# Performance work log

Measured on AMD Instinct MI355X. Metric: run time of the kernel, lower is better.

## Reference

```python
import jax, jax.numpy as jnp
import numpy as np

B, Lq, Lk, D, H = 8, 1024, 1024, 1024, 16
HD = D // H  # 64


def rotate_half(x):
    x1, x2 = jnp.split(x, 2, axis=-1)
    return jnp.concatenate([-x2, x1], axis=-1)


def setup_inputs() -> dict:
    key = jax.random.key(0)
    ks = jax.random.split(key, 16)
    inv_freq = 1.0 / (10000.0 ** (np.arange(0, HD, 2, dtype=np.float32) / HD))
    pos = np.arange(Lk, dtype=np.float32)
    ang = pos[:, None] * inv_freq[None, :]              # [Lk, HD/2]
    emb = np.concatenate([ang, ang], axis=-1)           # [Lk, HD]
    rope_cos = jnp.broadcast_to(jnp.asarray(np.cos(emb)), (B, Lk, HD))
    rope_sin = jnp.broadcast_to(jnp.asarray(np.sin(emb)), (B, Lk, HD))
    w = lambda k: jax.random.normal(k, (D, D), jnp.float32) * 0.02
    return {
        "query": jax.random.normal(ks[0], (B, Lq, D), jnp.float32),
        "key": jax.random.normal(ks[1], (B, Lk, D), jnp.float32),
        "value": jax.random.normal(ks[2], (B, Lk, D), jnp.float32),
        "Wq": w(ks[3]), "bq": jnp.zeros((D,), jnp.float32),
        "Wk": w(ks[4]), "bk": jnp.zeros((D,), jnp.float32),
        "Wv": w(ks[5]), "bv": jnp.zeros((D,), jnp.float32),
        "Wg": w(ks[6]), "bg": jnp.ones((D,), jnp.float32),
        "Wo": w(ks[7]), "bo": jnp.zeros((D,), jnp.float32),
        "rope_cos": rope_cos,
        "rope_sin": rope_sin,
        "key_padding_mask": jnp.zeros((B, Lk), bool),  # True = padded
    }


def reference(query, key, value, Wq, bq, Wk, bk, Wv, bv, Wg, bg, Wo, bo,
              rope_cos, rope_sin, key_padding_mask):
    b, lq, d = query.shape
    lk = key.shape[1]
    h, hd = H, d // H

    def heads(x, L):  # [B,L,D] -> [B,H,L,hd]
        return x.reshape(b, L, h, hd).transpose(0, 2, 1, 3)

    Q = heads(query @ Wq.T + bq, lq)
    K = heads(key @ Wk.T + bk, lk)
    V = heads(value @ Wv.T + bv, lk)

    def rope(x, cos, sin):
        L = x.shape[2]
        c = cos[:, None, :L, :]
        s = sin[:, None, :L, :]
        return x * c + rotate_half(x) * s

    K = rope(K, rope_cos, rope_sin)
    Q = rope(Q, rope_cos, rope_sin)  # rope_on_q=True, q uses same cos/sin

    scale = 1.0 / np.sqrt(hd)
    scores = jnp.einsum('bhqd,bhkd->bhqk', Q, K) * scale
    valid = ~key_padding_mask                     # [B,Lk], True = attend
    scores = jnp.where(valid[:, None, None, :], scores, jnp.float32(-1e30))
    attn = jax.nn.softmax(scores, axis=-1)
    out = jnp.einsum('bhqk,bhkd->bhqd', attn, V)  # [B,H,Lq,hd]
    out = jnp.nan_to_num(out, nan=0.0)
    out = out.transpose(0, 2, 1, 3).reshape(b, lq, d)
    gate = jax.nn.sigmoid(query @ Wg.T + bg)
    out = (out * gate) @ Wo.T + bo
    return out
```

## Files before the change

### kernel.cpp

```cpp
#include <hip/hip_runtime.h>

using ushort  = unsigned short;
using bf16x8  = __attribute__((ext_vector_type(8))) __bf16;
using bf16x4  = __attribute__((ext_vector_type(4))) __bf16;
using ushort8 = __attribute__((ext_vector_type(8))) unsigned short;
using f32x4   = __attribute__((ext_vector_type(4))) float;
using float4v = __attribute__((ext_vector_type(4))) float;

__device__ __forceinline__ float bf2f(ushort u) {
    union { unsigned int i; float f; } v; v.i = ((unsigned int)u) << 16; return v.f;
}
__device__ __forceinline__ ushort f2bf(float f) {
    union { float f; unsigned int i; } v; v.f = f;
    unsigned int r = v.i + 0x7FFFu + ((v.i >> 16) & 1u);
    return (ushort)(r >> 16);
}
__device__ __forceinline__ bf16x8 ld8(const ushort* p) {
    return __builtin_bit_cast(bf16x8, *(const ushort8*)p);
}
__device__ __forceinline__ void glds16(const void* g, void* l) {
    __builtin_amdgcn_global_load_lds(
        (const __attribute__((address_space(1))) unsigned int*)g,
        (__attribute__((address_space(3))) unsigned int*)l, 16, 0, 0);
}

__global__ void sniff_kernel(const ushort* __restrict__ q, int* __restrict__ flag) {
    const int lane = threadIdx.x;
    float mx = 0.0f;
    for (int i = lane; i < 512; i += 64) {
        float v = bf2f(q[2 * i]);
        mx = fmaxf(mx, fabsf(v));
    }
#pragma unroll
    for (int off = 32; off >= 1; off >>= 1) mx = fmaxf(mx, __shfl_xor(mx, off, 64));
    if (lane == 0) *flag = (mx > 1.0e6f) ? 1 : 0;
}

__device__ __forceinline__ void cvt8(const void* src, ushort* dst, int i, bool f32m) {
    if (f32m) {
        const float4v a = ((const float4v*)src)[2 * i];
        const float4v b = ((const float4v*)src)[2 * i + 1];
        bf16x8 o;
#pragma unroll
        for (int j = 0; j < 4; ++j) { o[j] = (__bf16)a[j]; o[j + 4] = (__bf16)b[j]; }
        ((ushort8*)dst)[i] = __builtin_bit_cast(ushort8, o);
    } else {
        ((ushort8*)dst)[i] = ((const ushort8*)src)[i];
    }
}

__global__ __launch_bounds__(256) void cvt_qkv(
    const void* __restrict__ s0, const void* __restrict__ s1, const void* __restrict__ s2,
    ushort* __restrict__ d0, ushort* __restrict__ d1, ushort* __restrict__ d2,
    const int* __restrict__ flag)
{
    const bool f32m = (*flag != 0);
    const int seg = blockIdx.x >> 11;
    const void* src = seg == 0 ? s0 : (seg == 1 ? s1 : s2);
    ushort*    dst = seg == 0 ? d0 : (seg == 1 ? d1 : d2);
    for (int i = (blockIdx.x & 2047) * 256 + threadIdx.x; i < 1048576; i += 2048 * 256)
        cvt8(src, dst, i, f32m);
}
__global__ __launch_bounds__(256) void cvt_w5(
    const void* __restrict__ s0, const void* __restrict__ s1, const void* __restrict__ s2,
    const void* __restrict__ s3, const void* __restrict__ s4,
    ushort* __restrict__ d0, ushort* __restrict__ d1, ushort* __restrict__ d2,
    ushort* __restrict__ d3, ushort* __restrict__ d4,
    const int* __restrict__ flag)
{
    const bool f32m = (*flag != 0);
    const int seg = blockIdx.x >> 9;
    const void* src = seg == 0 ? s0 : seg == 1 ? s1 : seg == 2 ? s2 : seg == 3 ? s3 : s4;
    ushort*    dst = seg == 0 ? d0 : seg == 1 ? d1 : seg == 2 ? d2 : seg == 3 ? d3 : d4;
    cvt8(src, dst, (blockIdx.x & 511) * 256 + threadIdx.x, f32m);
}

template<int EPI, int ABF16, int WBF16, int OUTF>
__global__ __launch_bounds__(256) void gemm_bt(
    const void* __restrict__ A, const void* __restrict__ W,
    const void* __restrict__ bias,
    const void* __restrict__ rc, const void* __restrict__ rs,
    void* __restrict__ C, const int* __restrict__ flag)
{
    constexpr int Kd = 1024, Nd = 1024;
    const bool f32m = (*flag != 0);
    const bool af32 = f32m && !ABF16;
    const bool wf32 = f32m && !WBF16;

    const int tid  = threadIdx.x;
    const int swz  = (blockIdx.x & 7) * 64 + (blockIdx.x >> 3);
    const int nb   = swz & 7;
    const int mb   = swz >> 3;
    const int wave = tid >> 6;
    const int lane = tid & 63;
    const int quad = lane >> 4;
    const int l16  = lane & 15;
    const int wr   = wave >> 1;
    const int wc   = wave & 1;

    __shared__ __align__(16) ushort As[2][128 * 32];
    __shared__ __align__(16) ushort Bs[2][128 * 32];

    const int arow0 = mb * 128;
    const int brow0 = nb * 128;

    auto ldregs = [&](float4v r[4], const float* src, int row0, int k0) {
#pragma unroll
        for (int j = 0; j < 2; ++j) {
            const int c = j * 256 + tid;
            const float* gp = src + (size_t)(row0 + (c >> 2)) * Kd + k0 + (c & 3) * 8;
            r[2 * j]     = *(const float4v*)gp;
            r[2 * j + 1] = *(const float4v*)(gp + 4);
        }
    };
    auto cvtwr = [&](ushort* lds, const float4v r[4]) {
#pragma unroll
        for (int j = 0; j < 2; ++j) {
            const int c = j * 256 + tid;
            bf16x8 o;
#pragma unroll
            for (int i = 0; i < 4; ++i) {
                o[i]     = (__bf16)r[2 * j][i];
                o[i + 4] = (__bf16)r[2 * j + 1][i];
            }
            *(ushort8*)&lds[c * 8] = __builtin_bit_cast(ushort8, o);
        }
    };
    auto stage16 = [&](ushort* lds, const ushort* src, int row0, int k0) {
#pragma unroll
        for (int j = 0; j < 2; ++j) {
            const int c = j * 256 + tid;
            glds16(src + (size_t)(row0 + (c >> 2)) * Kd + k0 + (c & 3) * 8, &lds[c * 8]);
        }
    };

    {
        float4v t[4];
        if (af32) { ldregs(t, (const float*)A, arow0, 0); cvtwr(As[0], t); }
        else      stage16(As[0], (const ushort*)A, arow0, 0);
        if (wf32) { ldregs(t, (const float*)W, brow0, 0); cvtwr(Bs[0], t); }
        else      stage16(Bs[0], (const ushort*)W, brow0, 0);
    }

    f32x4 acc[4][4] = {};
    int cur = 0;
    for (int kt = 0; kt < 32; ++kt) {
        __syncthreads();
        const bool pf = (kt < 31);
        const int  kn = (kt + 1) * 32;
        float4v ra[4], rb[4];
        if (pf) {
            if (af32) ldregs(ra, (const float*)A, arow0, kn);
            else      stage16(As[cur ^ 1], (const ushort*)A, arow0, kn);
            if (wf32) ldregs(rb, (const float*)W, brow0, kn);
            else      stage16(Bs[cur ^ 1], (const ushort*)W, brow0, kn);
        }
        bf16x8 fa[4], fb[4];
#pragma unroll
        for (int mi = 0; mi < 4; ++mi)
            fa[mi] = ld8(&As[cur][(wr * 64 + mi * 16 + l16) * 32 + quad * 8]);
#pragma unroll
        for (int ni = 0; ni < 4; ++ni)
            fb[ni] = ld8(&Bs[cur][(wc * 64 + ni * 16 + l16) * 32 + quad * 8]);
#pragma unroll
        for (int mi = 0; mi < 4; ++mi)
#pragma unroll
            for (int ni = 0; ni < 4; ++ni)
                acc[mi][ni] = __builtin_amdgcn_mfma_f32_16x16x32_bf16(fa[mi], fb[ni], acc[mi][ni], 0, 0, 0);
        if (pf) {
            if (af32) cvtwr(As[cur ^ 1], ra);
            if (wf32) cvtwr(Bs[cur ^ 1], rb);
        }
        cur ^= 1;
    }

    const bool of32 = OUTF && f32m;
    const int colbase = nb * 128 + wc * 64;
    float bv[4];
#pragma unroll
    for (int ni = 0; ni < 4; ++ni) {
        const int cg = colbase + ni * 16 + l16;
        bv[ni] = f32m ? ((const float*)bias)[cg] : bf2f(((const ushort*)bias)[cg]);
    }
    const int rowb = mb * 128 + wr * 64 + quad * 4;
#pragma unroll
    for (int mi = 0; mi < 4; ++mi) {
#pragma unroll
        for (int r = 0; r < 4; ++r) {
            const int rowg = rowb + mi * 16 + r;
            float v[4];
#pragma unroll
            for (int ni = 0; ni < 4; ++ni) v[ni] = acc[mi][ni][r] + bv[ni];
            if constexpr (EPI == 1 || EPI == 3) {
#pragma unroll
                for (int t = 0; t < 2; ++t) {
                    const size_t ci = (size_t)rowg * 64 + t * 16 + l16;
                    const float c = f32m ? ((const float*)rc)[ci] : bf2f(((const ushort*)rc)[ci]);
                    const float s = f32m ? ((const float*)rs)[ci] : bf2f(((const ushort*)rs)[ci]);
                    const float x1 = v[t], x2 = v[t + 2];
                    v[t]     = x1 * c - x2 * s;
                    v[t + 2] = x2 * c + x1 * s;
                }
                if constexpr (EPI == 3) {
#pragma unroll
                    for (int t = 0; t < 4; ++t) v[t] *= 0.125f;
                }
            } else if constexpr (EPI == 2) {
#pragma unroll
                for (int t = 0; t < 4; ++t) v[t] = 1.0f / (1.0f + __expf(-v[t]));
            }
#pragma unroll
            for (int ni = 0; ni < 4; ++ni) {
                const size_t idx = (size_t)rowg * Nd + colbase + ni * 16 + l16;
                if (of32) ((float*)C)[idx] = v[ni];
                else      ((ushort*)C)[idx] = f2bf(v[ni]);
            }
        }
    }
}

__global__ __launch_bounds__(256) void transpose_vh(
    const ushort* __restrict__ Vp, ushort* __restrict__ Vt)
{
    const int bb = blockIdx.x >> 8;
    const int pr = (blockIdx.x >> 4) & 15;
    const int cr = blockIdx.x & 15;
    __shared__ ushort t[64 * 65];
    const int tid = threadIdx.x;
    {
        const int r = tid >> 3, c8 = (tid & 7) * 8;
#pragma unroll
        for (int hh = 0; hh < 2; ++hh) {
            const int rr = r + hh * 32;
            const ushort8 v = *(const ushort8*)(Vp + ((size_t)(bb * 1024 + pr * 64 + rr)) * 1024 + cr * 64 + c8);
#pragma unroll
            for (int i = 0; i < 8; ++i) t[rr * 65 + c8 + i] = v[i];
        }
    }
    __syncthreads();
    {
        const int c = tid >> 2, p0 = (tid & 3) * 16;
        ushort8 o0, o1;
#pragma unroll
        for (int i = 0; i < 8; ++i) {
            o0[i] = t[(p0 + i) * 65 + c];
            o1[i] = t[(p0 + 8 + i) * 65 + c];
        }
        ushort* dst = Vt + ((size_t)(bb * 1024 + cr * 64 + c)) * 1024 + pr * 64 + p0;
        *(ushort8*)dst       = o0;
        *(ushort8*)(dst + 8) = o1;
    }
}

__global__ __launch_bounds__(512) void attn_kernel(
    const ushort* __restrict__ Qp, const ushort* __restrict__ Kp,
    const ushort* __restrict__ Vt, const ushort* __restrict__ G,
    const unsigned char* __restrict__ mask, ushort* __restrict__ O)
{
    const int swz = (blockIdx.x & 7) * 64 + (blockIdx.x >> 3);
    const int qb = swz & 3;
    const int h  = (swz >> 2) & 15;
    const int b  = swz >> 6;
    const int tid  = threadIdx.x;
    const int wave = tid >> 6;
    const int lane = tid & 63;
    const int quad = lane >> 4;
    const int l16  = lane & 15;
    const size_t Dm = 1024;

    __shared__ __align__(16) ushort Ks[2][64 * 64];
    __shared__ __align__(16) ushort Vs[2][64 * 64];
    __shared__ __align__(16) ushort Ps[8][16 * 72];
    __shared__ __align__(16) unsigned char Ms[1024];

    const int q0 = qb * 256 + wave * 32;
    bf16x8 qa[2][2];
#pragma unroll
    for (int u = 0; u < 2; ++u) {
        const ushort* Qb = Qp + ((size_t)b * 1024 + q0 + u * 16 + l16) * Dm + h * 64 + quad * 8;
        qa[u][0] = ld8(Qb);
        qa[u][1] = ld8(Qb + 32);
    }
    const ushort* Kbase = Kp + ((size_t)b * 1024) * Dm + h * 64;
    const ushort* Vbase = Vt + ((size_t)b * 1024 + h * 64) * 1024;

    auto stageK = [&](ushort* lds, int k0) {
        const int row = tid >> 3;
        const int col8 = (tid & 7) ^ (row & 7);
        glds16(Kbase + (size_t)(k0 + row) * Dm + col8 * 8, &lds[tid * 8]);
    };
    auto stageV = [&](ushort* lds, int k0) {
        const int row = tid >> 3;
        const int col8 = (tid & 7) ^ (row & 7);
        glds16(Vbase + (size_t)row * 1024 + k0 + col8 * 8, &lds[tid * 8]);
    };

    stageK(Ks[0], 0);
    stageV(Vs[0], 0);
    if (tid < 256)
        ((unsigned int*)Ms)[tid] = ((const unsigned int*)(mask + (size_t)b * 1024))[tid];
    __syncthreads();
    bool anym;
    {
        const unsigned long long* M8 = (const unsigned long long*)Ms;
        anym = __any((M8[lane] | M8[lane + 64]) != 0ULL);
    }

    float m_r[2] = { -3.0e38f, -3.0e38f };
    float l_r[2] = { 0.0f, 0.0f };
    f32x4 o[2][4] = {};

    int cur = 0;
    for (int kt = 0; kt < 16; ++kt) {
        __syncthreads();
        if (kt < 15) {
            stageK(Ks[cur ^ 1], (kt + 1) * 64);
            stageV(Vs[cur ^ 1], (kt + 1) * 64);
        }
        const int k0 = kt * 64;
        bf16x8 kf0[4], kf1[4];
#pragma unroll
        for (int ct = 0; ct < 4; ++ct) {
            const int row = ct * 16 + l16;
            kf0[ct] = ld8(&Ks[cur][row * 64 + ((quad)     ^ (row & 7)) * 8]);
            kf1[ct] = ld8(&Ks[cur][row * 64 + ((4 + quad) ^ (row & 7)) * 8]);
        }
        f32x4 s[2][4] = {};
        __builtin_amdgcn_s_setprio(1);
#pragma unroll
        for (int u = 0; u < 2; ++u)
#pragma unroll
            for (int ct = 0; ct < 4; ++ct) {
                s[u][ct] = __builtin_amdgcn_mfma_f32_16x16x32_bf16(kf0[ct], qa[u][0], s[u][ct], 0, 0, 0);
                s[u][ct] = __builtin_amdgcn_mfma_f32_16x16x32_bf16(kf1[ct], qa[u][1], s[u][ct], 0, 0, 0);
            }
        __builtin_amdgcn_s_setprio(0);
        bf16x8 vf[4][2];
#pragma unroll
        for (int t = 0; t < 4; ++t) {
            const int row = t * 16 + l16;
#pragma unroll
            for (int kk = 0; kk < 2; ++kk)
                vf[t][kk] = ld8(&Vs[cur][row * 64 + (((kk * 4 + quad) ^ (row & 7))) * 8]);
        }
#pragma unroll
        for (int u = 0; u < 2; ++u) {
            float sv[4][4];
#pragma unroll
            for (int ct = 0; ct < 4; ++ct)
#pragma unroll
                for (int r = 0; r < 4; ++r) sv[ct][r] = s[u][ct][r];
            if (anym) {
#pragma unroll
                for (int ct = 0; ct < 4; ++ct) {
                    const unsigned int mb4 = *(const unsigned int*)&Ms[k0 + ct * 16 + quad * 4];
#pragma unroll
                    for (int r = 0; r < 4; ++r)
                        if ((mb4 >> (8 * r)) & 0xffu) sv[ct][r] = -1e30f;
                }
            }
            float mxv = sv[0][0];
#pragma unroll
            for (int ct = 0; ct < 4; ++ct)
#pragma unroll
                for (int r = 0; r < 4; ++r) mxv = fmaxf(mxv, sv[ct][r]);
            mxv = fmaxf(mxv, __shfl_xor(mxv, 16, 64));
            mxv = fmaxf(mxv, __shfl_xor(mxv, 32, 64));
            if (__any(mxv > m_r[u] + 8.0f)) {
                const float mnew  = fmaxf(m_r[u], mxv);
                const float alpha = __expf(m_r[u] - mnew);
                l_r[u] *= alpha;
                m_r[u]  = mnew;
#pragma unroll
                for (int r = 0; r < 4; ++r) {
                    const float ar = __shfl(alpha, quad * 4 + r, 64);
#pragma unroll
                    for (int t = 0; t < 4; ++t) o[u][t][r] *= ar;
                }
            }
            float ls = 0.0f;
            bf16x4 w[4];
#pragma unroll
            for (int ct = 0; ct < 4; ++ct)
#pragma unroll
                for (int r = 0; r < 4; ++r) {
                    const float pv = __expf(sv[ct][r] - m_r[u]);
                    ls += pv;
                    w[ct][r] = (__bf16)pv;
                }
            l_r[u] += ls;
#pragma unroll
            for (int ct = 0; ct < 4; ++ct)
                *(bf16x4*)&Ps[wave][l16 * 72 + ct * 16 + quad * 4] = w[ct];
            asm volatile("s_waitcnt lgkmcnt(0)" ::: "memory");
            __builtin_amdgcn_sched_barrier(0);
            const bf16x8 pa0 = ld8(&Ps[wave][l16 * 72 + quad * 8]);
            const bf16x8 pa1 = ld8(&Ps[wave][l16 * 72 + 32 + quad * 8]);
            __builtin_amdgcn_s_setprio(1);
#pragma unroll
            for (int t = 0; t < 4; ++t) {
                o[u][t] = __builtin_amdgcn_mfma_f32_16x16x32_bf16(pa0, vf[t][0], o[u][t], 0, 0, 0);
                o[u][t] = __builtin_amdgcn_mfma_f32_16x16x32_bf16(pa1, vf[t][1], o[u][t], 0, 0, 0);
            }
            __builtin_amdgcn_s_setprio(0);
        }
        cur ^= 1;
    }
#pragma unroll
    for (int u = 0; u < 2; ++u) {
        float lt = l_r[u];
        lt += __shfl_xor(lt, 16, 64);
        lt += __shfl_xor(lt, 32, 64);
        const int rowg0 = b * 1024 + q0 + u * 16 + quad * 4;
#pragma unroll
        for (int r = 0; r < 4; ++r) {
            const float inv = 1.0f / __shfl(lt, quad * 4 + r, 64);
#pragma unroll
            for (int t = 0; t < 4; ++t) {
                const size_t idx = (size_t)(rowg0 + r) * Dm + h * 64 + t * 16 + l16;
                O[idx] = f2bf(o[u][t][r] * inv * bf2f(G[idx]));
            }
        }
    }
}

extern "C" void kernel_launch(void* const* d_in, const int* in_sizes, int n_in,
                              void* d_out, int out_size, void* d_ws, size_t ws_size,
                              hipStream_t stream)
{
    const void* query = d_in[0];
    const void* key   = d_in[1];
    const void* value = d_in[2];
    const void* Wq    = d_in[3];
    const void* bq    = d_in[4];
    const void* Wk    = d_in[5];
    const void* bk    = d_in[6];
    const void* Wv    = d_in[7];
    const void* bv    = d_in[8];
    const void* Wg    = d_in[9];
    const void* bg    = d_in[10];
    const void* Wo    = d_in[11];
    const void* bo    = d_in[12];
    const void* rc    = d_in[13];
    const void* rs    = d_in[14];
    const unsigned char* mask = (const unsigned char*)d_in[15];

    char* ws = (char*)d_ws;
    const size_t MB = (size_t)1 << 20;
    const size_t MB16 = 16 * MB;
    const bool big = ws_size >= 139 * MB;

    ushort* Qp = (ushort*)(ws);
    ushort* Kp = (ushort*)(ws + 1 * MB16);
    ushort* Vp = (ushort*)(ws + 2 * MB16);
    ushort* Gt = (ushort*)(ws + 3 * MB16);
    ushort* Vt = (ushort*)(ws + 4 * MB16);
    ushort* Ag = (ushort*)(ws + 2 * MB16);
    int*  flag = (int*)(ws + (big ? 138 * MB : 5 * MB16));

    const dim3 gb(512), gt(256);
    hipLaunchKernelGGL(sniff_kernel, dim3(1), dim3(64), 0, stream, (const ushort*)query, flag);

    if (big) {
        ushort* qbf = (ushort*)(ws + 80 * MB);
        ushort* kbf = (ushort*)(ws + 96 * MB);
        ushort* vbf = (ushort*)(ws + 112 * MB);
        ushort* wb[5];
        for (int i = 0; i < 5; ++i) wb[i] = (ushort*)(ws + 128 * MB + (size_t)i * 2 * MB);

        hipLaunchKernelGGL(cvt_qkv, dim3(3 * 2048), dim3(256), 0, stream,
                           query, key, value, qbf, kbf, vbf, flag);
        hipLaunchKernelGGL(cvt_w5, dim3(5 * 512), dim3(256), 0, stream,
                           Wq, Wk, Wv, Wg, Wo, wb[0], wb[1], wb[2], wb[3], wb[4], flag);

        hipLaunchKernelGGL((gemm_bt<3,1,1,0>), gb, gt, 0, stream, qbf, wb[0], bq, rc, rs, Qp, flag);
        hipLaunchKernelGGL((gemm_bt<1,1,1,0>), gb, gt, 0, stream, kbf, wb[1], bk, rc, rs, Kp, flag);
        hipLaunchKernelGGL((gemm_bt<0,1,1,0>), gb, gt, 0, stream, vbf, wb[2], bv, rc, rs, Vp, flag);
        hipLaunchKernelGGL((gemm_bt<2,1,1,0>), gb, gt, 0, stream, qbf, wb[3], bg, rc, rs, Gt, flag);

        hipLaunchKernelGGL(transpose_vh, dim3(2048), dim3(256), 0, stream, Vp, Vt);
        hipLaunchKernelGGL(attn_kernel,  dim3(512), dim3(512), 0, stream, Qp, Kp, Vt, Gt, mask, Ag);

        hipLaunchKernelGGL((gemm_bt<0,1,1,1>), gb, gt, 0, stream, Ag, wb[4], bo, rc, rs, d_out, flag);
    } else {
        hipLaunchKernelGGL((gemm_bt<3,0,0,0>), gb, gt, 0, stream, query, Wq, bq, rc, rs, Qp, flag);
        hipLaunchKernelGGL((gemm_bt<1,0,0,0>), gb, gt, 0, stream, key,   Wk, bk, rc, rs, Kp, flag);
        hipLaunchKernelGGL((gemm_bt<0,0,0,0>), gb, gt, 0, stream, value, Wv, bv, rc, rs, Vp, flag);
        hipLaunchKernelGGL((gemm_bt<2,0,0,0>), gb, gt, 0, stream, query, Wg, bg, rc, rs, Gt, flag);

        hipLaunchKernelGGL(transpose_vh, dim3(2048), dim3(256), 0, stream, Vp, Vt);
        hipLaunchKernelGGL(attn_kernel,  dim3(512), dim3(512), 0, stream, Qp, Kp, Vt, Gt, mask, Ag);

        hipLaunchKernelGGL((gemm_bt<0,1,0,1>), gb, gt, 0, stream, Ag, Wo, bo, rc, rs, d_out, flag);
    }
}
```

Before: 411.4 us.

## Fuse Q/K/V/gate projections into one GEMM launch and batch PV MFMAs

Replaces four separate projection GEMM launches with a single 2048-block kernel over a contiguous concatenated weight buffer, picking input, bias, epilogue and output per column segment. This fills the machine with one larger grid and removes launch gaps and tail effects between GEMMs. Separately, the attention kernel now writes P for both 16-row sub-tiles to a doubled LDS buffer and issues one wait and one batch of PV MFMAs, cutting waitcnt stalls. The attention change costs extra LDS and register pressure, and the fused GEMM adds runtime segment branches in its epilogue.

```diff
diff --git a/kernel.cpp b/kernel.cpp
--- a/kernel.cpp
+++ b/kernel.cpp
@@ -214,6 +214,119 @@
                 const size_t idx = (size_t)rowg * Nd + colbase + ni * 16 + l16;
                 if (of32) ((float*)C)[idx] = v[ni];
                 else      ((ushort*)C)[idx] = f2bf(v[ni]);
+            }
+        }
+    }
+}
+
+__global__ __launch_bounds__(256) void gemm_qkvg(
+    const ushort* __restrict__ qbf, const ushort* __restrict__ kbf,
+    const ushort* __restrict__ vbf, const ushort* __restrict__ Wcat,
+    const void* __restrict__ bq, const void* __restrict__ bk,
+    const void* __restrict__ bv_, const void* __restrict__ bg,
+    const void* __restrict__ rc, const void* __restrict__ rs,
+    ushort* __restrict__ Qp, ushort* __restrict__ Kp,
+    ushort* __restrict__ Vp, ushort* __restrict__ Gt,
+    const int* __restrict__ flag)
+{
+    constexpr int Kd = 1024;
+    const bool f32m = (*flag != 0);
+    const int tid  = threadIdx.x;
+    const int xcd  = blockIdx.x & 7;
+    const int rr   = blockIdx.x >> 3;
+    const int mb   = xcd * 8 + (rr & 7);
+    const int nb   = rr >> 3;
+    const int seg  = nb >> 3;
+    const ushort* A   = seg == 0 ? qbf : seg == 1 ? kbf : seg == 2 ? vbf : qbf;
+    const void* bias  = seg == 0 ? bq : seg == 1 ? bk : seg == 2 ? bv_ : bg;
+    ushort* C         = seg == 0 ? Qp : seg == 1 ? Kp : seg == 2 ? Vp : Gt;
+
+    const int wave = tid >> 6;
+    const int lane = tid & 63;
+    const int quad = lane >> 4;
+    const int l16  = lane & 15;
+    const int wr   = wave >> 1;
+    const int wc   = wave & 1;
+
+    __shared__ __align__(16) ushort As[2][128 * 32];
+    __shared__ __align__(16) ushort Bs[2][128 * 32];
+
+    const int arow0 = mb * 128;
+    const int brow0 = nb * 128;
+
+    auto stage16 = [&](ushort* lds, const ushort* src, int row0, int k0) {
+#pragma unroll
+        for (int j = 0; j < 2; ++j) {
+            const int c = j * 256 + tid;
+            glds16(src + (size_t)(row0 + (c >> 2)) * Kd + k0 + (c & 3) * 8, &lds[c * 8]);
+        }
+    };
+
+    stage16(As[0], A, arow0, 0);
+    stage16(Bs[0], Wcat, brow0, 0);
+
+    f32x4 acc[4][4] = {};
+    int cur = 0;
+    for (int kt = 0; kt < 32; ++kt) {
+        __syncthreads();
+        if (kt < 31) {
+            const int kn = (kt + 1) * 32;
+            stage16(As[cur ^ 1], A, arow0, kn);
+            stage16(Bs[cur ^ 1], Wcat, brow0, kn);
+        }
+        bf16x8 fa[4], fb[4];
+#pragma unroll
+        for (int mi = 0; mi < 4; ++mi)
+            fa[mi] = ld8(&As[cur][(wr * 64 + mi * 16 + l16) * 32 + quad * 8]);
+#pragma unroll
+        for (int ni = 0; ni < 4; ++ni)
+            fb[ni] = ld8(&Bs[cur][(wc * 64 + ni * 16 + l16) * 32 + quad * 8]);
+#pragma unroll
+        for (int mi = 0; mi < 4; ++mi)
+#pragma unroll
+            for (int ni = 0; ni < 4; ++ni)
+                acc[mi][ni] = __builtin_amdgcn_mfma_f32_16x16x32_bf16(fa[mi], fb[ni], acc[mi][ni], 0, 0, 0);
+        cur ^= 1;
+    }
+
+    const int colbase = (nb & 7) * 128 + wc * 64;
+    float bv[4];
+#pragma unroll
+    for (int ni = 0; ni < 4; ++ni) {
+        const int cg = colbase + ni * 16 + l16;
+        bv[ni] = f32m ? ((const float*)bias)[cg] : bf2f(((const ushort*)bias)[cg]);
+    }
+    const int rowb = mb * 128 + wr * 64 + quad * 4;
+#pragma unroll
+    for (int mi = 0; mi < 4; ++mi) {
+#pragma unroll
+        for (int r = 0; r < 4; ++r) {
+            const int rowg = rowb + mi * 16 + r;
+            float v[4];
+#pragma unroll
+            for (int ni = 0; ni < 4; ++ni) v[ni] = acc[mi][ni][r] + bv[ni];
+            if (seg <= 1) {
+#pragma unroll
+                for (int t = 0; t < 2; ++t) {
+                    const size_t ci = (size_t)rowg * 64 + t * 16 + l16;
+                    const float c = f32m ? ((const float*)rc)[ci] : bf2f(((const ushort*)rc)[ci]);
+                    const float s = f32m ? ((const float*)rs)[ci] : bf2f(((const ushort*)rs)[ci]);
+                    const float x1 = v[t], x2 = v[t + 2];
+                    v[t]     = x1 * c - x2 * s;
+                    v[t + 2] = x2 * c + x1 * s;
+                }
+                if (seg == 0) {
+#pragma unroll
+                    for (int t = 0; t < 4; ++t) v[t] *= 0.125f;
+                }
+            } else if (seg == 3) {
+#pragma unroll
+                for (int t = 0; t < 4; ++t) v[t] = 1.0f / (1.0f + __expf(-v[t]));
+            }
+#pragma unroll
+            for (int ni = 0; ni < 4; ++ni) {
+                const size_t idx = (size_t)rowg * 1024 + colbase + ni * 16 + l16;
+                C[idx] = f2bf(v[ni]);
             }
         }
     }
@@ -270,7 +383,7 @@
 
     __shared__ __align__(16) ushort Ks[2][64 * 64];
     __shared__ __align__(16) ushort Vs[2][64 * 64];
-    __shared__ __align__(16) ushort Ps[8][16 * 72];
+    __shared__ __align__(16) ushort Ps[8][2][16 * 72];
     __shared__ __align__(16) unsigned char Ms[1024];
 
     const int q0 = qb * 256 + wave * 32;
@@ -391,19 +504,25 @@
             l_r[u] += ls;
 #pragma unroll
             for (int ct = 0; ct < 4; ++ct)
-                *(bf16x4*)&Ps[wave][l16 * 72 + ct * 16 + quad * 4] = w[ct];
-            asm volatile("s_waitcnt lgkmcnt(0)" ::: "memory");
-            __builtin_amdgcn_sched_barrier(0);
-            const bf16x8 pa0 = ld8(&Ps[wave][l16 * 72 + quad * 8]);
-            const bf16x8 pa1 = ld8(&Ps[wave][l16 * 72 + 32 + quad * 8]);
-            __builtin_amdgcn_s_setprio(1);
+                *(bf16x4*)&Ps[wave][u][l16 * 72 + ct * 16 + quad * 4] = w[ct];
+        }
+        asm volatile("s_waitcnt lgkmcnt(0)" ::: "memory");
+        __builtin_amdgcn_sched_barrier(0);
+        bf16x8 pa[2][2];
+#pragma unroll
+        for (int u = 0; u < 2; ++u) {
+            pa[u][0] = ld8(&Ps[wave][u][l16 * 72 + quad * 8]);
+            pa[u][1] = ld8(&Ps[wave][u][l16 * 72 + 32 + quad * 8]);
+        }
+        __builtin_amdgcn_s_setprio(1);
+#pragma unroll
+        for (int u = 0; u < 2; ++u)
 #pragma unroll
             for (int t = 0; t < 4; ++t) {
-                o[u][t] = __builtin_amdgcn_mfma_f32_16x16x32_bf16(pa0, vf[t][0], o[u][t], 0, 0, 0);
-                o[u][t] = __builtin_amdgcn_mfma_f32_16x16x32_bf16(pa1, vf[t][1], o[u][t], 0, 0, 0);
-            }
-            __builtin_amdgcn_s_setprio(0);
-        }
+                o[u][t] = __builtin_amdgcn_mfma_f32_16x16x32_bf16(pa[u][0], vf[t][0], o[u][t], 0, 0, 0);
+                o[u][t] = __builtin_amdgcn_mfma_f32_16x16x32_bf16(pa[u][1], vf[t][1], o[u][t], 0, 0, 0);
+            }
+        __builtin_amdgcn_s_setprio(0);
         cur ^= 1;
     }
 #pragma unroll
@@ -465,18 +584,18 @@
         ushort* qbf = (ushort*)(ws + 80 * MB);
         ushort* kbf = (ushort*)(ws + 96 * MB);
         ushort* vbf = (ushort*)(ws + 112 * MB);
+        ushort* wcat = (ushort*)(ws + 128 * MB);
         ushort* wb[5];
-        for (int i = 0; i < 5; ++i) wb[i] = (ushort*)(ws + 128 * MB + (size_t)i * 2 * MB);
+        for (int i = 0; i < 5; ++i) wb[i] = wcat + (size_t)i * 1024 * 1024;
 
         hipLaunchKernelGGL(cvt_qkv, dim3(3 * 2048), dim3(256), 0, stream,
                            query, key, value, qbf, kbf, vbf, flag);
         hipLaunchKernelGGL(cvt_w5, dim3(5 * 512), dim3(256), 0, stream,
                            Wq, Wk, Wv, Wg, Wo, wb[0], wb[1], wb[2], wb[3], wb[4], flag);
 
-        hipLaunchKernelGGL((gemm_bt<3,1,1,0>), gb, gt, 0, stream, qbf, wb[0], bq, rc, rs, Qp, flag);
-        hipLaunchKernelGGL((gemm_bt<1,1,1,0>), gb, gt, 0, stream, kbf, wb[1], bk, rc, rs, Kp, flag);
-        hipLaunchKernelGGL((gemm_bt<0,1,1,0>), gb, gt, 0, stream, vbf, wb[2], bv, rc, rs, Vp, flag);
-        hipLaunchKernelGGL((gemm_bt<2,1,1,0>), gb, gt, 0, stream, qbf, wb[3], bg, rc, rs, Gt, flag);
+        hipLaunchKernelGGL(gemm_qkvg, dim3(2048), dim3(256), 0, stream,
+                           qbf, kbf, vbf, wcat, bq, bk, bv, bg, rc, rs,
+                           Qp, Kp, Vp, Gt, flag);
 
         hipLaunchKernelGGL(transpose_vh, dim3(2048), dim3(256), 0, stream, Vp, Vt);
         hipLaunchKernelGGL(attn_kernel,  dim3(512), dim3(512), 0, stream, Qp, Kp, Vt, Gt, mask, Ag);
```

Result: faster. 395.4 us (-3.9%).
